# Performance work log

Hardware: AMD Instinct MI355X
Metric: run time of the kernel (lower is better)

The kernel has to match this reference:

```python
import jax, jax.numpy as jnp
import numpy as np

D_MODEL = 256
SCALE = 1.0 / np.sqrt(D_MODEL).astype(np.float32)


def setup_inputs() -> dict:
    key = jax.random.key(0)
    ks = jax.random.split(key, 8)
    B, M, d = 32, 8192, D_MODEL
    lim = 1.0 / np.sqrt(d)  # torch Linear default init range
    inp = {
        "query": jax.random.normal(ks[0], (B, d), dtype=jnp.float32),
        "tokens": jax.random.normal(ks[1], (B, M, d), dtype=jnp.float32),
        "q_w": jax.random.uniform(ks[2], (d, d), jnp.float32, -lim, lim),
        "q_b": jax.random.uniform(ks[3], (d,), jnp.float32, -lim, lim),
        "k_w": jax.random.uniform(ks[4], (d, d), jnp.float32, -lim, lim),
        "k_b": jax.random.uniform(ks[5], (d,), jnp.float32, -lim, lim),
        "v_w": jax.random.uniform(ks[6], (d, d), jnp.float32, -lim, lim),
        "v_b": jax.random.uniform(ks[7], (d,), jnp.float32, -lim, lim),
    }
    return inp


def reference(query, tokens, q_w, q_b, k_w, k_b, v_w, v_b):
    # q: [B, d]; k, v: [B, M, d]  (torch Linear: x @ W.T + b)
    q = query @ q_w.T + q_b
    k = tokens @ k_w.T + k_b
    v = tokens @ v_w.T + v_b
    # single-query scores: [B, M]
    logits = jnp.einsum("bd,bmd->bm", q, k) * SCALE
    w = jax.nn.softmax(logits, axis=-1)
    # weighted sum over tokens -> [B, d]
    return jnp.einsum("bm,bmd->bd", w, v)
```

## Files before the change

kernel.cpp:

```cpp
#include <hip/hip_runtime.h>
#include <math.h>

#define BB 32
#define MM 8192
#define DD 256
#define SCALE 0.0625f
#define WPB 128
#define TPW (MM / WPB)
#define BLK_PER_B (WPB / 4)

using f4 = __attribute__((ext_vector_type(4))) float;

__global__ __launch_bounds__(256) void k_qr(
    const float* __restrict__ query, const float* __restrict__ q_w,
    const float* __restrict__ q_b, const float* __restrict__ k_w,
    const float* __restrict__ v_w, float* __restrict__ vwt,
    float* __restrict__ r)
{
    const int tid = threadIdx.x;
    if (blockIdx.x >= BB) {
        const int t  = blockIdx.x - BB;
        const int dj = tid & 31;
        const int e8 = tid >> 5;
        const int d  = t * 32 + dj;
        #pragma unroll 4
        for (int it = 0; it < 32; ++it) {
            const int e = it * 8 + e8;
            vwt[e * DD + d] = v_w[d * DD + e];
        }
        return;
    }

    const int b = blockIdx.x;
    __shared__ float qv[DD];
    __shared__ float qp[DD];
    qv[tid] = query[b * DD + tid];
    __syncthreads();
    float acc = q_b[tid];
    const float* qwrow = q_w + (size_t)tid * DD;
    #pragma unroll 8
    for (int e = 0; e < DD; ++e) acc += qv[e] * qwrow[e];
    qp[tid] = acc;
    __syncthreads();
    float racc = 0.f;
    #pragma unroll 8
    for (int d = 0; d < DD; ++d) racc += qp[d] * k_w[d * DD + tid];
    r[b * DD + tid] = racc * SCALE;
}

__global__ __launch_bounds__(256) void k_flash(
    const float* __restrict__ tokens, const float* __restrict__ r,
    float* __restrict__ part_m, float* __restrict__ part_l,
    f4* __restrict__ part_u)
{
    const int b    = blockIdx.y;
    const int blk  = blockIdx.x;
    const int tid  = threadIdx.x;
    const int w    = tid >> 6;
    const int lane = tid & 63;
    const int g    = lane & 15;
    const int tg   = lane >> 4;
    const int wi   = blk * 4 + w;
    const int m0   = wi * TPW;

    const f4* r4 = (const f4*)(r + b * DD);
    f4 rr[4];
    #pragma unroll
    for (int c = 0; c < 4; ++c) rr[c] = r4[16 * c + g];

    const f4* tok = (const f4*)tokens + ((size_t)b * MM + m0) * (DD / 4)
                  + (size_t)tg * (DD / 4) + g;

    float mw = -INFINITY, lw = 0.f;
    f4 u[4] = {{0,0,0,0},{0,0,0,0},{0,0,0,0},{0,0,0,0}};

    f4 xn[4];
    #pragma unroll
    for (int c = 0; c < 4; ++c)
        xn[c] = __builtin_nontemporal_load(tok + 16 * c);

    const int NIT = TPW / 4;
    for (int it = 0; it < NIT; ++it) {
        f4 x[4];
        #pragma unroll
        for (int c = 0; c < 4; ++c) x[c] = xn[c];

        if (it + 1 < NIT) {
            const f4* nxt = tok + (size_t)(it + 1) * 4 * (DD / 4);
            #pragma unroll
            for (int c = 0; c < 4; ++c)
                xn[c] = __builtin_nontemporal_load(nxt + 16 * c);
        }

        float s0 = x[0].x*rr[0].x + x[0].y*rr[0].y + x[0].z*rr[0].z + x[0].w*rr[0].w;
        float s1 = x[1].x*rr[1].x + x[1].y*rr[1].y + x[1].z*rr[1].z + x[1].w*rr[1].w;
        float s2 = x[2].x*rr[2].x + x[2].y*rr[2].y + x[2].z*rr[2].z + x[2].w*rr[2].w;
        float s3 = x[3].x*rr[3].x + x[3].y*rr[3].y + x[3].z*rr[3].z + x[3].w*rr[3].w;
        float p  = (s0 + s1) + (s2 + s3);

        p += __shfl_xor(p, 1);
        p += __shfl_xor(p, 2);
        p += __shfl_xor(p, 4);
        p += __shfl_xor(p, 8);

        const float newm  = fmaxf(mw, p);
        const float alpha = __expf(mw - newm);
        const float wj    = __expf(p  - newm);
        mw = newm;
        lw = lw * alpha + wj;
        #pragma unroll
        for (int c = 0; c < 4; ++c) {
            u[c].x = u[c].x * alpha + wj * x[c].x;
            u[c].y = u[c].y * alpha + wj * x[c].y;
            u[c].z = u[c].z * alpha + wj * x[c].z;
            u[c].w = u[c].w * alpha + wj * x[c].w;
        }
    }

    float gm = mw;
    gm = fmaxf(gm, __shfl_xor(gm, 16));
    gm = fmaxf(gm, __shfl_xor(gm, 32));
    const float beta = __expf(mw - gm);
    float L = lw * beta;
    L += __shfl_xor(L, 16);
    L += __shfl_xor(L, 32);
    #pragma unroll
    for (int c = 0; c < 4; ++c) {
        u[c].x *= beta; u[c].y *= beta; u[c].z *= beta; u[c].w *= beta;
        u[c].x += __shfl_xor(u[c].x, 16);
        u[c].y += __shfl_xor(u[c].y, 16);
        u[c].z += __shfl_xor(u[c].z, 16);
        u[c].w += __shfl_xor(u[c].w, 16);
        u[c].x += __shfl_xor(u[c].x, 32);
        u[c].y += __shfl_xor(u[c].y, 32);
        u[c].z += __shfl_xor(u[c].z, 32);
        u[c].w += __shfl_xor(u[c].w, 32);
    }

    const int pi = b * WPB + wi;
    if (lane == 0) { part_m[pi] = gm; part_l[pi] = L; }
    f4 val = u[0];
    val = (tg == 1) ? u[1] : val;
    val = (tg == 2) ? u[2] : val;
    val = (tg == 3) ? u[3] : val;
    part_u[(size_t)pi * 64 + lane] = val;
}

__global__ __launch_bounds__(256) void k_combine(
    const float* __restrict__ part_m, const float* __restrict__ part_l,
    const f4* __restrict__ part_u, const float* __restrict__ vwt,
    const float* __restrict__ v_b, float* __restrict__ out)
{
    const int b = blockIdx.x, tid = threadIdx.x;
    __shared__ float red[256];
    __shared__ float sf[WPB];
    __shared__ f4 suh[4][64];
    __shared__ float su[DD];

    const float pm = (tid < WPB) ? part_m[b * WPB + tid] : -INFINITY;
    red[tid] = pm;
    __syncthreads();
    #pragma unroll
    for (int s = 128; s > 0; s >>= 1) {
        if (tid < s) red[tid] = fmaxf(red[tid], red[tid + s]);
        __syncthreads();
    }
    const float gm = red[0];
    __syncthreads();

    float lterm = 0.f;
    if (tid < WPB) {
        const float f = __expf(pm - gm);
        sf[tid] = f;
        lterm = part_l[b * WPB + tid] * f;
    }
    red[tid] = lterm;
    __syncthreads();
    #pragma unroll
    for (int s = 128; s > 0; s >>= 1) {
        if (tid < s) red[tid] += red[tid + s];
        __syncthreads();
    }
    const float l = red[0];

    const int slot = tid & 63;
    const int rg   = tid >> 6;
    const f4* pu = part_u + (size_t)b * WPB * 64;
    f4 acc = {0.f, 0.f, 0.f, 0.f};
    #pragma unroll 8
    for (int i = rg; i < WPB; i += 4)
        acc += pu[(size_t)i * 64 + slot] * sf[i];
    suh[rg][slot] = acc;
    __syncthreads();
    if (tid < 64) {
        f4 s = suh[0][tid] + suh[1][tid] + suh[2][tid] + suh[3][tid];
        s *= (1.f / l);
        ((f4*)su)[tid] = s;
    }
    __syncthreads();

    float o = v_b[tid];
    #pragma unroll 8
    for (int e = 0; e < DD; ++e) o += su[e] * vwt[e * DD + tid];
    out[b * DD + tid] = o;
}

extern "C" void kernel_launch(void* const* d_in, const int* in_sizes, int n_in,
                              void* d_out, int out_size, void* d_ws, size_t ws_size,
                              hipStream_t stream) {
    const float* query  = (const float*)d_in[0];
    const float* tokens = (const float*)d_in[1];
    const float* q_w    = (const float*)d_in[2];
    const float* q_b    = (const float*)d_in[3];
    const float* k_w    = (const float*)d_in[4];
    const float* v_w    = (const float*)d_in[6];
    const float* v_b    = (const float*)d_in[7];
    float* out = (float*)d_out;

    float* ws     = (float*)d_ws;
    float* r      = ws;
    float* part_m = r + BB * DD;
    float* part_l = part_m + BB * WPB;
    float* part_u = part_l + BB * WPB;
    float* vwt    = part_u + (size_t)BB * WPB * DD;

    k_qr<<<dim3(BB + 8), dim3(256), 0, stream>>>(query, q_w, q_b, k_w,
                                                 v_w, vwt, r);
    k_flash<<<dim3(BLK_PER_B, BB), dim3(256), 0, stream>>>(
        tokens, r, part_m, part_l, (f4*)part_u);
    k_combine<<<dim3(BB), dim3(256), 0, stream>>>(
        part_m, part_l, (const f4*)part_u, vwt, v_b, out);
}
```

Before: 392.7 us.

## Deepen token prefetch to two stages, halve wave splits, vectorize q projection

```diff
diff --git a/kernel.cpp b/kernel.cpp
--- a/kernel.cpp
+++ b/kernel.cpp
@@ -5,7 +5,7 @@
 #define MM 8192
 #define DD 256
 #define SCALE 0.0625f
-#define WPB 128
+#define WPB 64
 #define TPW (MM / WPB)
 #define BLK_PER_B (WPB / 4)
 
@@ -32,14 +32,18 @@
     }
 
     const int b = blockIdx.x;
-    __shared__ float qv[DD];
+    __shared__ __align__(16) float qv[DD];
     __shared__ float qp[DD];
     qv[tid] = query[b * DD + tid];
     __syncthreads();
     float acc = q_b[tid];
-    const float* qwrow = q_w + (size_t)tid * DD;
-    #pragma unroll 8
-    for (int e = 0; e < DD; ++e) acc += qv[e] * qwrow[e];
+    const f4* qw4 = (const f4*)(q_w + (size_t)tid * DD);
+    const f4* qv4 = (const f4*)qv;
+    #pragma unroll 8
+    for (int e = 0; e < DD / 4; ++e) {
+        const f4 a = qv4[e], w = qw4[e];
+        acc += a.x * w.x + a.y * w.y + a.z * w.z + a.w * w.w;
+    }
     qp[tid] = acc;
     __syncthreads();
     float racc = 0.f;
@@ -48,7 +52,7 @@
     r[b * DD + tid] = racc * SCALE;
 }
 
-__global__ __launch_bounds__(256) void k_flash(
+__global__ __launch_bounds__(256, 2) void k_flash(
     const float* __restrict__ tokens, const float* __restrict__ r,
     float* __restrict__ part_m, float* __restrict__ part_l,
     f4* __restrict__ part_u)
@@ -74,24 +78,7 @@
     float mw = -INFINITY, lw = 0.f;
     f4 u[4] = {{0,0,0,0},{0,0,0,0},{0,0,0,0},{0,0,0,0}};
 
-    f4 xn[4];
-    #pragma unroll
-    for (int c = 0; c < 4; ++c)
-        xn[c] = __builtin_nontemporal_load(tok + 16 * c);
-
-    const int NIT = TPW / 4;
-    for (int it = 0; it < NIT; ++it) {
-        f4 x[4];
-        #pragma unroll
-        for (int c = 0; c < 4; ++c) x[c] = xn[c];
-
-        if (it + 1 < NIT) {
-            const f4* nxt = tok + (size_t)(it + 1) * 4 * (DD / 4);
-            #pragma unroll
-            for (int c = 0; c < 4; ++c)
-                xn[c] = __builtin_nontemporal_load(nxt + 16 * c);
-        }
-
+    auto body = [&](const f4* x) {
         float s0 = x[0].x*rr[0].x + x[0].y*rr[0].y + x[0].z*rr[0].z + x[0].w*rr[0].w;
         float s1 = x[1].x*rr[1].x + x[1].y*rr[1].y + x[1].z*rr[1].z + x[1].w*rr[1].w;
         float s2 = x[2].x*rr[2].x + x[2].y*rr[2].y + x[2].z*rr[2].z + x[2].w*rr[2].w;
@@ -115,6 +102,41 @@
             u[c].z = u[c].z * alpha + wj * x[c].z;
             u[c].w = u[c].w * alpha + wj * x[c].w;
         }
+    };
+
+    const int NIT = TPW / 4;
+    f4 xa[4], xb[4];
+    #pragma unroll
+    for (int c = 0; c < 4; ++c)
+        xa[c] = __builtin_nontemporal_load(tok + 16 * c);
+    {
+        const f4* t1 = tok + 4 * (DD / 4);
+        #pragma unroll
+        for (int c = 0; c < 4; ++c)
+            xb[c] = __builtin_nontemporal_load(t1 + 16 * c);
+    }
+
+    for (int it = 0; it < NIT; it += 2) {
+        f4 x[4];
+        #pragma unroll
+        for (int c = 0; c < 4; ++c) x[c] = xa[c];
+        if (it + 2 < NIT) {
+            const f4* nxt = tok + (size_t)(it + 2) * 4 * (DD / 4);
+            #pragma unroll
+            for (int c = 0; c < 4; ++c)
+                xa[c] = __builtin_nontemporal_load(nxt + 16 * c);
+        }
+        body(x);
+
+        #pragma unroll
+        for (int c = 0; c < 4; ++c) x[c] = xb[c];
+        if (it + 3 < NIT) {
+            const f4* nxt = tok + (size_t)(it + 3) * 4 * (DD / 4);
+            #pragma unroll
+            for (int c = 0; c < 4; ++c)
+                xb[c] = __builtin_nontemporal_load(nxt + 16 * c);
+        }
+        body(x);
     }
 
     float gm = mw;
@@ -155,7 +177,7 @@
     __shared__ float red[256];
     __shared__ float sf[WPB];
     __shared__ f4 suh[4][64];
-    __shared__ float su[DD];
+    __shared__ __align__(16) float su[DD];
 
     const float pm = (tid < WPB) ? part_m[b * WPB + tid] : -INFINITY;
     red[tid] = pm;
```

New measurement: 388.0 us. No clear change (-1.2%).
